# Performance work log

Hardware: AMD Instinct MI355X
Metric: run time of the kernel (lower is better)

The kernel has to match this reference:

```python
import jax, jax.numpy as jnp
import numpy as np

B, C, H, W = 32, 1024, 32, 32  # N = H*W must equal C for the attn_c * attn_s broadcast
C8 = C // 8


def setup_inputs() -> dict:
    key = jax.random.key(0)
    ks = jax.random.split(key, 9)
    s = 1.0 / np.sqrt(C)
    return {
        "z": jax.random.normal(ks[0], (B, C, H, W), jnp.float32),
        "x": jax.random.normal(ks[1], (B, C, H, W), jnp.float32),
        "y": jax.random.normal(ks[2], (B, C, H, W), jnp.float32),
        "Wq": jax.random.normal(ks[3], (C8, C), jnp.float32) * s,
        "bq": jax.random.normal(ks[4], (C8,), jnp.float32) * 0.01,
        "Wk": jax.random.normal(ks[5], (C8, C), jnp.float32) * s,
        "bk": jax.random.normal(ks[6], (C8,), jnp.float32) * 0.01,
        "Wv": jax.random.normal(ks[7], (C, C), jnp.float32) * s,
        "bv": jax.random.normal(ks[8], (C,), jnp.float32) * 0.01,
    }


def reference(z, x, y, Wq, bq, Wk, bk, Wv, bv):
    b, c, h, w = x.shape
    n = h * w
    xf = x.reshape(b, c, n)
    yf = y.reshape(b, c, n)
    zf = z.reshape(b, c, n)

    # 1x1 convs == channel matmuls
    q = jnp.einsum('oc,bcn->bon', Wq, xf) + bq[None, :, None]   # (B, C/8, N)
    k = jnp.einsum('oc,bcn->bon', Wk, yf) + bk[None, :, None]   # (B, C/8, N)

    # channel-projected spatial attention: (B, N, N)
    energy_c = jnp.einsum('bcn,bcm->bnm', q, k)
    attention_c = jax.nn.softmax(energy_c, axis=-1)

    # raw channel attention: (B, C, C)
    energy_s = jnp.einsum('bcn,bdn->bcd', xf, yf)
    energy_s = jnp.max(energy_s, axis=-1, keepdims=True) - energy_s
    attention_s = jax.nn.softmax(energy_s, axis=-1)

    # multiplicative combine + third softmax (requires N == C)
    attention = jax.nn.softmax(attention_c * attention_s, axis=-1)

    v = jnp.einsum('oc,bcn->bon', Wv, zf) + bv[None, :, None]   # (B, C, N)
    # out[b,c,m] = sum_n v[b,c,n] * attention[b,m,n]  (value @ attention^T)
    out = jnp.einsum('bcn,bmn->bcm', v, attention)
    return z + out.reshape(b, c, h, w)
```

## Files before the change

### kernel.cpp

```cpp
#include <hip/hip_runtime.h>
#include <hip/hip_bf16.h>

typedef __attribute__((ext_vector_type(8))) short s8_t;
typedef __attribute__((ext_vector_type(4))) float f4_t;

__device__ __forceinline__ unsigned short f2bf(float f) {
  union { float f; unsigned u; } x; x.f = f;
  unsigned r = x.u + 0x7fffu + ((x.u >> 16) & 1u);
  return (unsigned short)(r >> 16);
}

__device__ __forceinline__ void split1(float v, unsigned short& h, unsigned short& l) {
  unsigned b = __float_as_uint(v);
  unsigned hb = b & 0xFFFF0000u;
  h = (unsigned short)(b >> 16);
  float lo = v - __uint_as_float(hb);
  l = (unsigned short)(__float_as_uint(lo) >> 16);
}

__device__ __forceinline__ void split2(float e0, float e1, unsigned& hp, unsigned& lp) {
  unsigned b0 = __float_as_uint(e0), b1 = __float_as_uint(e1);
  unsigned h0 = b0 & 0xFFFF0000u, h1 = b1 & 0xFFFF0000u;
  hp = (b0 >> 16) | h1;
  float l0 = e0 - __uint_as_float(h0), l1 = e1 - __uint_as_float(h1);
  lp = (__float_as_uint(l0) >> 16) | (__float_as_uint(l1) & 0xFFFF0000u);
}

__device__ __forceinline__ void gload16(const void* g, void* l) {
  __builtin_amdgcn_global_load_lds(
      (const __attribute__((address_space(1))) void*)g,
      (__attribute__((address_space(3))) void*)l, 16, 0, 0);
}

__device__ __forceinline__ void swz_grid(int& bx, int& by, int& bz) {
  const int gx = gridDim.x, gy = gridDim.y;
  const int nwg = gx * gy * gridDim.z;
  const int flat = (blockIdx.z * gy + blockIdx.y) * gx + blockIdx.x;
  const int s = (flat & 7) * (nwg >> 3) + (flat >> 3);
  bx = s % gx;
  const int r = s / gx;
  by = r % gy;
  bz = r / gy;
}

__global__ __launch_bounds__(256) void k_convert(const float* __restrict__ in,
                                                 unsigned short* __restrict__ out, int n) {
  int i = (blockIdx.x * 256 + threadIdx.x) * 8;
  if (i >= n) return;
  float4 a = *(const float4*)(in + i);
  float4 b = *(const float4*)(in + i + 4);
  ushort4 u0; u0.x = f2bf(a.x); u0.y = f2bf(a.y); u0.z = f2bf(a.z); u0.w = f2bf(a.w);
  ushort4 u1; u1.x = f2bf(b.x); u1.y = f2bf(b.y); u1.z = f2bf(b.z); u1.w = f2bf(b.w);
  *(ushort4*)(out + i) = u0;
  *(ushort4*)(out + i + 4) = u1;
}

__global__ __launch_bounds__(256) void k_tsplitT(const float* __restrict__ in,
                                                 unsigned short* __restrict__ th,
                                                 unsigned short* __restrict__ tl) {
  __shared__ float tile[64][65];
  const int t = threadIdx.x, bz = blockIdx.z;
  const int r0 = blockIdx.y * 64, c0 = blockIdx.x * 64;
  const float* ip = in + (size_t)bz * 1048576;
  const size_t ob = (size_t)bz * 1048576;
  const int tr = t >> 4, tc = (t & 15) * 4;
#pragma unroll
  for (int p = 0; p < 4; ++p) {
    int r = p * 16 + tr;
    float4 v = *(const float4*)(ip + (size_t)(r0 + r) * 1024 + c0 + tc);
    tile[r][tc] = v.x; tile[r][tc + 1] = v.y; tile[r][tc + 2] = v.z; tile[r][tc + 3] = v.w;
  }
  __syncthreads();
#pragma unroll
  for (int p = 0; p < 4; ++p) {
    int n = p * 16 + tr;
    float a = tile[tc][n], b = tile[tc + 1][n], c = tile[tc + 2][n], d = tile[tc + 3][n];
    ushort4 h, l;
    split1(a, h.x, l.x); split1(b, h.y, l.y); split1(c, h.z, l.z); split1(d, h.w, l.w);
    *(ushort4*)(th + ob + (size_t)(c0 + n) * 1024 + r0 + tc) = h;
    *(ushort4*)(tl + ob + (size_t)(c0 + n) * 1024 + r0 + tc) = l;
  }
}

__global__ __launch_bounds__(256) void k_transpbf(const float* __restrict__ in,
                                                  unsigned short* __restrict__ outt) {
  __shared__ unsigned short tile[64][72];
  const int t = threadIdx.x, b = blockIdx.z;
  const int r0 = blockIdx.y * 64, c0 = blockIdx.x * 64;
  const float* ip = in + (size_t)b * 1048576;
  const int tr = t >> 4, tc = (t & 15) * 4;
#pragma unroll
  for (int p = 0; p < 4; ++p) {
    int r = p * 16 + tr;
    float4 v = *(const float4*)(ip + (size_t)(r0 + r) * 1024 + c0 + tc);
    tile[r][tc] = f2bf(v.x); tile[r][tc + 1] = f2bf(v.y);
    tile[r][tc + 2] = f2bf(v.z); tile[r][tc + 3] = f2bf(v.w);
  }
  __syncthreads();
#pragma unroll
  for (int p = 0; p < 4; ++p) {
    int n = p * 16 + tr;
    ushort4 w;
    w.x = tile[tc][n]; w.y = tile[tc + 1][n]; w.z = tile[tc + 2][n]; w.w = tile[tc + 3][n];
    *(ushort4*)(outt + (size_t)b * 1048576 + (size_t)(c0 + n) * 1024 + r0 + tc) = w;
  }
}

__device__ __forceinline__ void split_write_swz(unsigned short* buf, int w0, int w1,
                                                const float* av, const float* bv) {
  unsigned ah[8], al[8], bh[8], bl[8];
#pragma unroll
  for (int p = 0; p < 8; ++p) {
    split2(av[2 * p], av[2 * p + 1], ah[p], al[p]);
    split2(bv[2 * p], bv[2 * p + 1], bh[p], bl[p]);
  }
  *(uint4*)(buf + w0) = *(uint4*)(ah);
  *(uint4*)(buf + w1) = *(uint4*)(ah + 4);
  *(uint4*)(buf + 4096 + w0) = *(uint4*)(al);
  *(uint4*)(buf + 4096 + w1) = *(uint4*)(al + 4);
  *(uint4*)(buf + 8192 + w0) = *(uint4*)(bh);
  *(uint4*)(buf + 8192 + w1) = *(uint4*)(bh + 4);
  *(uint4*)(buf + 12288 + w0) = *(uint4*)(bl);
  *(uint4*)(buf + 12288 + w1) = *(uint4*)(bl + 4);
}

template <int BIAS_MODE>
__global__ __launch_bounds__(256) void k_mfma3(
    const float* __restrict__ A, int lda, long long sA,
    const float* __restrict__ B, int ldb, long long sB,
    float* __restrict__ C, int ldc, long long sC,
    const float* __restrict__ bias, int K) {
  __shared__ __align__(16) unsigned short sm[16384];
  int bxs, bys, bz; swz_grid(bxs, bys, bz);
  const int tid = threadIdx.x;
  const int lane = tid & 63, wave = tid >> 6;
  const int wr = wave >> 1, wc = wave & 1;
  const int m0 = bxs * 128, n0 = bys * 128;

  const int sr = tid >> 1, sh = (tid & 1) * 16;
  const float* ag = A + (long long)bz * sA + (long long)(m0 + sr) * lda + sh;
  const float* bg = B + (long long)bz * sB + (long long)(n0 + sr) * ldb + sh;
  const int swm = (sr >> 1) & 3;
  const int s0 = (tid & 1) * 2;
  const int w0 = sr * 32 + (s0 ^ swm) * 8;
  const int w1 = sr * 32 + ((s0 + 1) ^ swm) * 8;

  const int lr = lane & 15, lg = lane >> 4;
  const int rdm = (lr >> 1) & 3;
  const int fa = (wr * 64 + lr) * 32 + (lg ^ rdm) * 8;
  const int fb = (wc * 64 + lr) * 32 + (lg ^ rdm) * 8;

  f4_t acc[4][4];
#pragma unroll
  for (int i = 0; i < 4; ++i)
#pragma unroll
    for (int j = 0; j < 4; ++j) acc[i][j] = (f4_t)0.f;

  for (int k0 = 0; k0 < K; k0 += 32) {
    float av[16], bv[16];
#pragma unroll
    for (int p = 0; p < 4; ++p) {
      *(float4*)(av + p * 4) = *(const float4*)(ag + p * 4);
      *(float4*)(bv + p * 4) = *(const float4*)(bg + p * 4);
    }
    split_write_swz(sm, w0, w1, av, bv);
    ag += 32; bg += 32;
    __syncthreads();
    const unsigned short* Ahp = sm;
    const unsigned short* Alp = sm + 4096;
    const unsigned short* Bhp = sm + 8192;
    const unsigned short* Blp = sm + 12288;
    s8_t fah[4], fbh[4], ftmp[4];
#pragma unroll
    for (int f = 0; f < 4; ++f) {
      fah[f] = *(const s8_t*)(Ahp + fa + f * 512);
      fbh[f] = *(const s8_t*)(Bhp + fb + f * 512);
    }
#pragma unroll
    for (int i = 0; i < 4; ++i)
#pragma unroll
      for (int j = 0; j < 4; ++j)
        acc[i][j] = __builtin_amdgcn_mfma_f32_16x16x32_bf16(fah[i], fbh[j], acc[i][j], 0, 0, 0);
#pragma unroll
    for (int f = 0; f < 4; ++f) ftmp[f] = *(const s8_t*)(Blp + fb + f * 512);
#pragma unroll
    for (int i = 0; i < 4; ++i)
#pragma unroll
      for (int j = 0; j < 4; ++j)
        acc[i][j] = __builtin_amdgcn_mfma_f32_16x16x32_bf16(fah[i], ftmp[j], acc[i][j], 0, 0, 0);
#pragma unroll
    for (int f = 0; f < 4; ++f) ftmp[f] = *(const s8_t*)(Alp + fa + f * 512);
#pragma unroll
    for (int i = 0; i < 4; ++i)
#pragma unroll
      for (int j = 0; j < 4; ++j)
        acc[i][j] = __builtin_amdgcn_mfma_f32_16x16x32_bf16(ftmp[i], fbh[j], acc[i][j], 0, 0, 0);
    __syncthreads();
  }

#pragma unroll
  for (int i = 0; i < 4; ++i) {
    const int rbase = m0 + wr * 64 + i * 16 + lg * 4;
#pragma unroll
    for (int j = 0; j < 4; ++j) {
      const int col = n0 + wc * 64 + j * 16 + lr;
      float bc = (BIAS_MODE == 2) ? bias[col] : 0.f;
#pragma unroll
      for (int e = 0; e < 4; ++e) {
        float v = acc[i][j][e];
        if (BIAS_MODE == 2) v += bc;
        C[(long long)bz * sC + (long long)(rbase + e) * ldc + col] = v;
      }
    }
  }
}

__global__ __launch_bounds__(256) void k_qk3p(
    const unsigned short* __restrict__ Axh, const unsigned short* __restrict__ Axl,
    const unsigned short* __restrict__ Ayh, const unsigned short* __restrict__ Ayl,
    const float* __restrict__ Wqf, const float* __restrict__ Wkf,
    const float* __restrict__ bqf, const float* __restrict__ bkf,
    float* __restrict__ Qt, float* __restrict__ Kt) {
  __shared__ __align__(16) unsigned short smAh[8192], smAl[8192];
  __shared__ __align__(16) unsigned short smBh[4096], smBl[4096];
  int bx, by, bz; swz_grid(bx, by, bz);
  const unsigned short* Ah = by ? Ayh : Axh;
  const unsigned short* Al = by ? Ayl : Axl;
  const float* Bf = by ? Wkf : Wqf;
  const float* bias = by ? bkf : bqf;
  float* Of = by ? Kt : Qt;

  const int tid = threadIdx.x, lane = tid & 63, wave = tid >> 6;
  const int wr = wave >> 1, wc = wave & 1;
  const int m0 = bx * 128;

  const int ch0 = wave * 64 + lane, ch1 = ch0 + 256;
  const int r0 = ch0 >> 2, kc0 = (((ch0 & 3) ^ ((ch0 >> 3) & 3))) * 8;
  const int r1 = ch1 >> 2, kc1 = (((ch1 & 3) ^ ((ch1 >> 3) & 3))) * 8;
  const unsigned short* pah0 = Ah + (long long)bz * 1048576 + (long long)(m0 + r0) * 1024 + kc0;
  const unsigned short* pah1 = Ah + (long long)bz * 1048576 + (long long)(m0 + r1) * 1024 + kc1;
  const unsigned short* pal0 = Al + (long long)bz * 1048576 + (long long)(m0 + r0) * 1024 + kc0;
  const unsigned short* pal1 = Al + (long long)bz * 1048576 + (long long)(m0 + r1) * 1024 + kc1;

  const int sr = tid >> 1, sh = (tid & 1) * 16;
  const float* bg = Bf + (long long)sr * 1024 + sh;
  const int swm = (sr >> 1) & 3;
  const int sB0 = (tid & 1) * 2;
  const int w0 = sr * 32 + (sB0 ^ swm) * 8;
  const int w1 = sr * 32 + ((sB0 + 1) ^ swm) * 8;

  const int lr = lane & 15, lg = lane >> 4;
  const int rdm = (lr >> 1) & 3;
  const int fa = (wr * 64 + lr) * 32 + (lg ^ rdm) * 8;
  const int fb = (wc * 64 + lr) * 32 + (lg ^ rdm) * 8;

  f4_t acc[4][4];
#pragma unroll
  for (int i = 0; i < 4; ++i)
#pragma unroll
    for (int j = 0; j < 4; ++j) acc[i][j] = (f4_t)0.f;

  float bv[16];
  auto stageA = [&](int b) {
    char* dh = (char*)smAh + b * 8192 + wave * 1024;
    char* dl = (char*)smAl + b * 8192 + wave * 1024;
    gload16(pah0, dh); gload16(pah1, dh + 4096);
    gload16(pal0, dl); gload16(pal1, dl + 4096);
    pah0 += 32; pah1 += 32; pal0 += 32; pal1 += 32;
  };
  auto loadW = [&]() {
#pragma unroll
    for (int p = 0; p < 4; ++p) *(float4*)(bv + p * 4) = *(const float4*)(bg + p * 4);
    bg += 32;
  };
  auto writeW = [&]() {
    unsigned bh[8], bl[8];
#pragma unroll
    for (int p = 0; p < 8; ++p) split2(bv[2 * p], bv[2 * p + 1], bh[p], bl[p]);
    *(uint4*)(smBh + w0) = *(uint4*)(bh);
    *(uint4*)(smBh + w1) = *(uint4*)(bh + 4);
    *(uint4*)(smBl + w0) = *(uint4*)(bl);
    *(uint4*)(smBl + w1) = *(uint4*)(bl + 4);
  };

  stageA(0);
  loadW();
  writeW();
  asm volatile("s_waitcnt vmcnt(0)" ::: "memory");
  __builtin_amdgcn_sched_barrier(0);
  __builtin_amdgcn_s_barrier();
  __builtin_amdgcn_sched_barrier(0);

  for (int t = 0; t < 32; ++t) {
    const bool more = (t < 31);
    if (more) { stageA((t + 1) & 1); loadW(); }
    const unsigned short* Ahp = smAh + (t & 1) * 4096;
    const unsigned short* Alp = smAl + (t & 1) * 4096;
    s8_t fah[4], fbh[4], ft[4];
#pragma unroll
    for (int f = 0; f < 4; ++f) {
      fah[f] = *(const s8_t*)(Ahp + fa + f * 512);
      fbh[f] = *(const s8_t*)(smBh + fb + f * 512);
    }
#pragma unroll
    for (int i = 0; i < 4; ++i)
#pragma unroll
      for (int j = 0; j < 4; ++j)
        acc[i][j] = __builtin_amdgcn_mfma_f32_16x16x32_bf16(fah[i], fbh[j], acc[i][j], 0, 0, 0);
#pragma unroll
    for (int f = 0; f < 4; ++f) ft[f] = *(const s8_t*)(smBl + fb + f * 512);
#pragma unroll
    for (int i = 0; i < 4; ++i)
#pragma unroll
      for (int j = 0; j < 4; ++j)
        acc[i][j] = __builtin_amdgcn_mfma_f32_16x16x32_bf16(fah[i], ft[j], acc[i][j], 0, 0, 0);
#pragma unroll
    for (int f = 0; f < 4; ++f) ft[f] = *(const s8_t*)(Alp + fa + f * 512);
#pragma unroll
    for (int i = 0; i < 4; ++i)
#pragma unroll
      for (int j = 0; j < 4; ++j)
        acc[i][j] = __builtin_amdgcn_mfma_f32_16x16x32_bf16(ft[i], fbh[j], acc[i][j], 0, 0, 0);
    __builtin_amdgcn_sched_barrier(0);
    __builtin_amdgcn_s_barrier();
    __builtin_amdgcn_sched_barrier(0);
    if (more) {
      writeW();
      asm volatile("s_waitcnt vmcnt(0)" ::: "memory");
    }
    __builtin_amdgcn_sched_barrier(0);
    __builtin_amdgcn_s_barrier();
    __builtin_amdgcn_sched_barrier(0);
  }

#pragma unroll
  for (int i = 0; i < 4; ++i) {
    const int rbase = m0 + wr * 64 + i * 16 + lg * 4;
#pragma unroll
    for (int j = 0; j < 4; ++j) {
      const int col = wc * 64 + j * 16 + lr;
      const float bc = bias[col];
#pragma unroll
      for (int e = 0; e < 4; ++e)
        Of[(long long)bz * 131072 + (long long)(rbase + e) * 128 + col] = acc[i][j][e] + bc;
    }
  }
}

template <int BIAS_MODE, bool OUT_BF16, bool RESID>
__global__ __launch_bounds__(512) void k_mfma256(
    const unsigned short* __restrict__ A, int lda, long long sA,
    const unsigned short* __restrict__ B, int ldb, long long sB,
    void* __restrict__ Cp, int ldc, long long sC,
    const float* __restrict__ bias,
    const float* __restrict__ resid, long long sR, int K) {
  __shared__ __align__(16) unsigned short As[32768];
  __shared__ __align__(16) unsigned short Bs[32768];
  int bxs, bys, bz; swz_grid(bxs, bys, bz);
  const int tid = threadIdx.x;
  const int lane = tid & 63, wave = tid >> 6;
  const int wr = wave >> 2, wc = wave & 3;
  const int m0 = bxs * 256, n0 = bys * 256;

  const int cA0 = tid, cA1 = tid + 512;
  const int rr0 = cA0 >> 2, sl0 = ((cA0 & 3) ^ ((cA0 >> 3) & 3)) * 8;
  const int rr1 = cA1 >> 2, sl1 = ((cA1 & 3) ^ ((cA1 >> 3) & 3)) * 8;
  const unsigned short* pa0 = A + (long long)bz * sA + (long long)(m0 + rr0) * lda + sl0;
  const unsigned short* pa1 = A + (long long)bz * sA + (long long)(m0 + rr1) * lda + sl1;
  const unsigned short* pb0 = B + (long long)bz * sB + (long long)(n0 + rr0) * ldb + sl0;
  const unsigned short* pb1 = B + (long long)bz * sB + (long long)(n0 + rr1) * ldb + sl1;

  const int lr = lane & 15, lg = lane >> 4;
  const int rdm = (lr >> 1) & 3;
  const int fa = (wr * 128 + lr) * 32 + (lg ^ rdm) * 8;
  const int fb = (wc * 64 + lr) * 32 + (lg ^ rdm) * 8;

  f4_t acc[8][4];
#pragma unroll
  for (int i = 0; i < 8; ++i)
#pragma unroll
    for (int j = 0; j < 4; ++j) acc[i][j] = (f4_t)0.f;

  unsigned short* a0 = As;        unsigned short* a1 = As + 8192;
  unsigned short* a2 = As + 16384; unsigned short* a3 = As + 24576;
  unsigned short* b0 = Bs;        unsigned short* b1 = Bs + 8192;
  unsigned short* b2 = Bs + 16384; unsigned short* b3 = Bs + 24576;

  auto stage = [&](unsigned short* la, unsigned short* lb) {
    gload16(pa0, (char*)la + wave * 1024);
    gload16(pa1, (char*)la + 8192 + wave * 1024);
    gload16(pb0, (char*)lb + wave * 1024);
    gload16(pb1, (char*)lb + 8192 + wave * 1024);
    pa0 += 32; pa1 += 32; pb0 += 32; pb1 += 32;
  };

  const int nt = K >> 5;
  stage(a0, b0);
  stage(a1, b1);
  stage(a2, b2);

  for (int t = 0; t < nt; ++t) {
    if (t + 3 < nt) {
      stage(a3, b3);
      asm volatile("s_waitcnt vmcnt(12)" ::: "memory");
    } else if (t + 2 < nt) {
      asm volatile("s_waitcnt vmcnt(8)" ::: "memory");
    } else if (t + 1 < nt) {
      asm volatile("s_waitcnt vmcnt(4)" ::: "memory");
    } else {
      asm volatile("s_waitcnt vmcnt(0)" ::: "memory");
    }
    __builtin_amdgcn_sched_barrier(0);
    __builtin_amdgcn_s_barrier();
    __builtin_amdgcn_sched_barrier(0);
    const unsigned short* ap = a0;
    const unsigned short* bp = b0;
    s8_t af[8], bf[4];
#pragma unroll
    for (int i = 0; i < 8; ++i) af[i] = *(const s8_t*)(ap + fa + i * 512);
#pragma unroll
    for (int j = 0; j < 4; ++j) bf[j] = *(const s8_t*)(bp + fb + j * 512);
#pragma unroll
    for (int i = 0; i < 8; ++i)
#pragma unroll
      for (int j = 0; j < 4; ++j)
        acc[i][j] = __builtin_amdgcn_mfma_f32_16x16x32_bf16(af[i], bf[j], acc[i][j], 0, 0, 0);
    __builtin_amdgcn_sched_barrier(0);
    __builtin_amdgcn_s_barrier();
    __builtin_amdgcn_sched_barrier(0);
    unsigned short* ta = a0; a0 = a1; a1 = a2; a2 = a3; a3 = ta;
    unsigned short* tb = b0; b0 = b1; b1 = b2; b2 = b3; b3 = tb;
  }

#pragma unroll
  for (int i = 0; i < 8; ++i) {
    const int rbase = m0 + wr * 128 + i * 16 + lg * 4;
#pragma unroll
    for (int j = 0; j < 4; ++j) {
      const int col = n0 + wc * 64 + j * 16 + lr;
#pragma unroll
      for (int e = 0; e < 4; ++e) {
        const int row = rbase + e;
        float v = acc[i][j][e];
        if (BIAS_MODE == 1) v += bias[row];
        const long long off = (long long)bz * sC + (long long)row * ldc + col;
        if (RESID) v += resid[(long long)bz * sR + (long long)row * ldc + col];
        if (OUT_BF16) ((unsigned short*)Cp)[off] = f2bf(v);
        else          ((float*)Cp)[off] = v;
      }
    }
  }
}

__device__ __forceinline__ float wred_max(float v) {
#pragma unroll
  for (int o = 1; o < 64; o <<= 1) v = fmaxf(v, __shfl_xor(v, o, 64));
  return v;
}
__device__ __forceinline__ float wred_sum(float v) {
#pragma unroll
  for (int o = 1; o < 64; o <<= 1) v += __shfl_xor(v, o, 64);
  return v;
}

__global__ __launch_bounds__(256) void k_combine(float* __restrict__ ec,
                                                 const float* __restrict__ es) {
  const int lane = threadIdx.x & 63, wid = threadIdx.x >> 6;
  const size_t row = (size_t)blockIdx.x * 4 + wid;
  float* cp = ec + row * 1024;
  const float* sp = es + row * 1024;
  float4 c[4], s[4];
#pragma unroll
  for (int p = 0; p < 4; ++p) {
    c[p] = ((const float4*)cp)[lane * 4 + p];
    s[p] = ((const float4*)sp)[lane * 4 + p];
  }
  float mx = -3.4e38f;
#pragma unroll
  for (int p = 0; p < 4; ++p)
    mx = fmaxf(mx, fmaxf(fmaxf(c[p].x, c[p].y), fmaxf(c[p].z, c[p].w)));
  mx = wred_max(mx);
  float e[16], lsum = 0.f;
#pragma unroll
  for (int p = 0; p < 4; ++p) {
    e[4 * p]     = __expf(c[p].x - mx);
    e[4 * p + 1] = __expf(c[p].y - mx);
    e[4 * p + 2] = __expf(c[p].z - mx);
    e[4 * p + 3] = __expf(c[p].w - mx);
    lsum += e[4 * p] + e[4 * p + 1] + e[4 * p + 2] + e[4 * p + 3];
  }
  const float sc = wred_sum(lsum);
  float mt = -3.4e38f;
#pragma unroll
  for (int p = 0; p < 4; ++p)
    mt = fmaxf(mt, fmaxf(fmaxf(-s[p].x, -s[p].y), fmaxf(-s[p].z, -s[p].w)));
  mt = wred_max(mt);
  float f[16]; lsum = 0.f;
#pragma unroll
  for (int p = 0; p < 4; ++p) {
    f[4 * p]     = __expf(-s[p].x - mt);
    f[4 * p + 1] = __expf(-s[p].y - mt);
    f[4 * p + 2] = __expf(-s[p].z - mt);
    f[4 * p + 3] = __expf(-s[p].w - mt);
    lsum += f[4 * p] + f[4 * p + 1] + f[4 * p + 2] + f[4 * p + 3];
  }
  const float ss = wred_sum(lsum);
  const float rc = 1.f / sc, rs = 1.f / ss;
  float g[16]; lsum = 0.f;
#pragma unroll
  for (int q = 0; q < 16; ++q) {
    g[q] = __expf((e[q] * rc) * (f[q] * rs));
    lsum += g[q];
  }
  const float s3 = wred_sum(lsum);
  const float r3 = 1.f / s3;
#pragma unroll
  for (int p = 0; p < 4; ++p) {
    ushort4 o;
    o.x = f2bf(g[4 * p] * r3);     o.y = f2bf(g[4 * p + 1] * r3);
    o.z = f2bf(g[4 * p + 2] * r3); o.w = f2bf(g[4 * p + 3] * r3);
    ((ushort4*)cp)[lane * 4 + p] = o;
  }
}

extern "C" void kernel_launch(void* const* d_in, const int* in_sizes, int n_in,
                              void* d_out, int out_size, void* d_ws, size_t ws_size,
                              hipStream_t stream) {
  const float* z = (const float*)d_in[0];
  const float* x = (const float*)d_in[1];
  const float* y = (const float*)d_in[2];
  const float* Wq = (const float*)d_in[3];
  const float* bq = (const float*)d_in[4];
  const float* Wk = (const float*)d_in[5];
  const float* bk = (const float*)d_in[6];
  const float* Wv = (const float*)d_in[7];
  const float* bv = (const float*)d_in[8];
  float* out = (float*)d_out;

  char* ws = (char*)d_ws;
  unsigned short* yth = (unsigned short*)ws;
  unsigned short* ytl = yth + 33554432;
  float* es = (float*)ws;
  unsigned short* z_t = (unsigned short*)ws;
  unsigned short* v_bf = z_t + 33554432;
  char* wsB = ws + 134217728;
  unsigned short* xth = (unsigned short*)wsB;
  unsigned short* xtl = xth + 33554432;
  float* ec = (float*)wsB;
  unsigned short* attn = (unsigned short*)wsB;
  char* wsC = ws + 268435456;
  float* q_t = (float*)wsC;
  float* k_t = q_t + 4194304;
  unsigned short* wv = (unsigned short*)wsC;

  dim3 blk(256);
  hipLaunchKernelGGL(k_tsplitT, dim3(16, 16, 32), blk, 0, stream, x, xth, xtl);
  hipLaunchKernelGGL(k_tsplitT, dim3(16, 16, 32), blk, 0, stream, y, yth, ytl);
  hipLaunchKernelGGL(k_qk3p, dim3(8, 2, 32), blk, 0, stream,
                     xth, xtl, yth, ytl, Wq, Wk, bq, bk, q_t, k_t);
  hipLaunchKernelGGL((k_mfma3<0>), dim3(8, 8, 32), blk, 0, stream,
                     x, 1024, 1048576LL, y, 1024, 1048576LL, es, 1024, 1048576LL,
                     (const float*)nullptr, 1024);
  hipLaunchKernelGGL((k_mfma3<0>), dim3(8, 8, 32), blk, 0, stream,
                     q_t, 128, 131072LL, k_t, 128, 131072LL, ec, 1024, 1048576LL,
                     (const float*)nullptr, 128);
  hipLaunchKernelGGL(k_combine, dim3(8192), blk, 0, stream, ec, es);
  hipLaunchKernelGGL(k_transpbf, dim3(16, 16, 32), blk, 0, stream, z, z_t);
  hipLaunchKernelGGL(k_convert, dim3(512), blk, 0, stream, Wv, wv, 1048576);
  hipLaunchKernelGGL((k_mfma256<1, true, false>), dim3(4, 4, 32), dim3(512), 0, stream,
                     wv, 1024, 0LL, z_t, 1024, 1048576LL, (void*)v_bf, 1024, 1048576LL,
                     bv, (const float*)nullptr, 0LL, 1024);
  hipLaunchKernelGGL((k_mfma256<0, false, true>), dim3(4, 4, 32), dim3(512), 0, stream,
                     v_bf, 1024, 1048576LL, attn, 2048, 2097152LL, (void*)out, 1024, 1048576LL,
                     (const float*)nullptr, z, 1048576LL, 1024);
}
```

Baseline: 786.2 us.

## Interleave prefetch loads with split MFMA phases and drop trailing barrier

After: 765.3 us. 2.7% less time.

```diff
diff --git a/kernel.cpp b/kernel.cpp
--- a/kernel.cpp
+++ b/kernel.cpp
@@ -386,48 +386,52 @@
   unsigned short* b0 = Bs;        unsigned short* b1 = Bs + 8192;
   unsigned short* b2 = Bs + 16384; unsigned short* b3 = Bs + 24576;
 
-  auto stage = [&](unsigned short* la, unsigned short* lb) {
-    gload16(pa0, (char*)la + wave * 1024);
-    gload16(pa1, (char*)la + 8192 + wave * 1024);
-    gload16(pb0, (char*)lb + wave * 1024);
-    gload16(pb1, (char*)lb + 8192 + wave * 1024);
-    pa0 += 32; pa1 += 32; pb0 += 32; pb1 += 32;
-  };
+  auto gA0 = [&](unsigned short* la) { gload16(pa0, (char*)la + wave * 1024); pa0 += 32; };
+  auto gA1 = [&](unsigned short* la) { gload16(pa1, (char*)la + 8192 + wave * 1024); pa1 += 32; };
+  auto gB0 = [&](unsigned short* lb) { gload16(pb0, (char*)lb + wave * 1024); pb0 += 32; };
+  auto gB1 = [&](unsigned short* lb) { gload16(pb1, (char*)lb + 8192 + wave * 1024); pb1 += 32; };
 
   const int nt = K >> 5;
-  stage(a0, b0);
-  stage(a1, b1);
-  stage(a2, b2);
+  gA0(a0); gA1(a0); gB0(b0); gB1(b0);
+  gA0(a1); gA1(a1); gB0(b1); gB1(b1);
+  gA0(a2); gA1(a2); gB0(b2); gB1(b2);
 
   for (int t = 0; t < nt; ++t) {
-    if (t + 3 < nt) {
-      stage(a3, b3);
-      asm volatile("s_waitcnt vmcnt(12)" ::: "memory");
-    } else if (t + 2 < nt) {
-      asm volatile("s_waitcnt vmcnt(8)" ::: "memory");
-    } else if (t + 1 < nt) {
-      asm volatile("s_waitcnt vmcnt(4)" ::: "memory");
-    } else {
-      asm volatile("s_waitcnt vmcnt(0)" ::: "memory");
-    }
+    const int rem = nt - 1 - t;
+    if (rem >= 2)      asm volatile("s_waitcnt vmcnt(8)" ::: "memory");
+    else if (rem == 1) asm volatile("s_waitcnt vmcnt(4)" ::: "memory");
+    else               asm volatile("s_waitcnt vmcnt(0)" ::: "memory");
     __builtin_amdgcn_sched_barrier(0);
     __builtin_amdgcn_s_barrier();
     __builtin_amdgcn_sched_barrier(0);
+    const bool pf = (t + 3 < nt);
     const unsigned short* ap = a0;
     const unsigned short* bp = b0;
-    s8_t af[8], bf[4];
-#pragma unroll
-    for (int i = 0; i < 8; ++i) af[i] = *(const s8_t*)(ap + fa + i * 512);
+    s8_t af[4], af2[4], bf[4];
+    if (pf) gA0(a3);
 #pragma unroll
     for (int j = 0; j < 4; ++j) bf[j] = *(const s8_t*)(bp + fb + j * 512);
-#pragma unroll
-    for (int i = 0; i < 8; ++i)
+    if (pf) gA1(a3);
+#pragma unroll
+    for (int i = 0; i < 4; ++i) af[i] = *(const s8_t*)(ap + fa + i * 512);
+    if (pf) gB0(b3);
+    __builtin_amdgcn_s_setprio(1);
+#pragma unroll
+    for (int i = 0; i < 4; ++i)
 #pragma unroll
       for (int j = 0; j < 4; ++j)
         acc[i][j] = __builtin_amdgcn_mfma_f32_16x16x32_bf16(af[i], bf[j], acc[i][j], 0, 0, 0);
-    __builtin_amdgcn_sched_barrier(0);
-    __builtin_amdgcn_s_barrier();
-    __builtin_amdgcn_sched_barrier(0);
+    __builtin_amdgcn_s_setprio(0);
+    if (pf) gB1(b3);
+#pragma unroll
+    for (int i = 0; i < 4; ++i) af2[i] = *(const s8_t*)(ap + fa + (i + 4) * 512);
+    __builtin_amdgcn_s_setprio(1);
+#pragma unroll
+    for (int i = 0; i < 4; ++i)
+#pragma unroll
+      for (int j = 0; j < 4; ++j)
+        acc[i + 4][j] = __builtin_amdgcn_mfma_f32_16x16x32_bf16(af2[i], bf[j], acc[i + 4][j], 0, 0, 0);
+    __builtin_amdgcn_s_setprio(0);
     unsigned short* ta = a0; a0 = a1; a1 = a2; a2 = a3; a3 = ta;
     unsigned short* tb = b0; b0 = b1; b1 = b2; b2 = b3; b3 = tb;
   }
```
